# Optimization experiments

Measured on AMD Instinct MI355X. Metric: run time of the kernel, lower is better.

The kernel has to match this reference:

```python
import jax, jax.numpy as jnp
import numpy as np

VOL_DIM = 256  # stored volume is [256,256,256,1]


def _deform(c, W1, b1, W2, b2, W3, b3, Wf, bf):
    # chain of 1x1x1 convs (== per-voxel matmuls) with cos activations, residual *5
    h = jnp.cos(jnp.einsum('...c,cd->...d', c, W1) + b1)
    h = jnp.cos(jnp.einsum('...c,cd->...d', h, W2) + b2)
    h = jnp.cos(jnp.einsum('...c,cd->...d', h, W3) + b3)
    return c + 5.0 * (jnp.einsum('...c,cd->...d', h, Wf) + bf)


def _trilinear_sample(vol, coords):
    # vol: [X,Y,Z,C]; coords: [...,3] in voxel units (identity nifti edges)
    X, Y, Z, _ = vol.shape
    hi = jnp.array([X - 1, Y - 1, Z - 1], dtype=coords.dtype)
    c = jnp.clip(coords, 0.0, hi)
    c0 = jnp.floor(c)
    f = c - c0
    i0 = c0.astype(jnp.int32)
    i1 = jnp.minimum(i0 + 1, jnp.array([X - 1, Y - 1, Z - 1], jnp.int32))
    x0, y0, z0 = i0[..., 0], i0[..., 1], i0[..., 2]
    x1, y1, z1 = i1[..., 0], i1[..., 1], i1[..., 2]
    fx, fy, fz = f[..., 0:1], f[..., 1:2], f[..., 2:3]
    gx, gy, gz = 1.0 - fx, 1.0 - fy, 1.0 - fz
    out = (vol[x0, y0, z0] * (gx * gy * gz) + vol[x1, y0, z0] * (fx * gy * gz)
         + vol[x0, y1, z0] * (gx * fy * gz) + vol[x0, y0, z1] * (gx * gy * fz)
         + vol[x1, y1, z0] * (fx * fy * gz) + vol[x1, y0, z1] * (fx * gy * fz)
         + vol[x0, y1, z1] * (gx * fy * fz) + vol[x1, y1, z1] * (fx * fy * fz))
    return out  # [...,C]


def setup_inputs() -> dict:
    key = jax.random.key(0)
    ks = jax.random.split(key, 12)
    B, P = 64, 32
    # coords in [0, 255] world==voxel units; extra intensity channel (unused by call)
    coords = jax.random.uniform(ks[0], (B, P, P, P, 3), jnp.float32) * (VOL_DIM - 1.0)
    inten = jax.random.normal(ks[1], (B, P, P, P, 1), jnp.float32)
    x = jnp.concatenate([coords, inten], axis=-1)
    s = 0.1
    return {
        'x': x,
        'W1': jax.random.normal(ks[2], (3, 32), jnp.float32) * s,
        'b1': jax.random.normal(ks[3], (32,), jnp.float32) * s,
        'W2': jax.random.normal(ks[4], (32, 32), jnp.float32) * s,
        'b2': jax.random.normal(ks[5], (32,), jnp.float32) * s,
        'W3': jax.random.normal(ks[6], (32, 32), jnp.float32) * s,
        'b3': jax.random.normal(ks[7], (32,), jnp.float32) * s,
        'Wf': jax.random.normal(ks[8], (32, 3), jnp.float32) * s,
        'bf': jax.random.normal(ks[9], (3,), jnp.float32) * s,
        'vol': jax.random.normal(ks[10], (VOL_DIM, VOL_DIM, VOL_DIM, 1), jnp.float32),
    }


def reference(x, W1, b1, W2, b2, W3, b3, Wf, bf, vol):
    c = x[..., 0:3]                                   # world coords
    c = _deform(c, W1, b1, W2, b2, W3, b3, Wf, bf)    # deformed coords
    return _trilinear_sample(vol, c)                  # [B,32,32,32,1]
```

## Files before the change

kernel.cpp:

```cpp
#include <hip/hip_runtime.h>


#define NPTS (64 * 32 * 32 * 32)
#define NBLK64 (NPTS / 64)
#define NBLK (NPTS / 256)
#define SSTR 40

#define BXN 86
#define BYN 128
#define BZN 86
#define NBRICK (BXN * BYN * BZN)
#define RETILE_T (NBRICK * 8)
#define RETILE_BLK (RETILE_T / 256)
#define HALO_BYTES ((size_t)NBRICK * 64)

#define NBRICK_F (86 * 256 * 86)
#define RETILE2_T (NBRICK_F * 4)
#define RETILE2_BLK (RETILE2_T / 256)
#define FULL_BYTES ((size_t)NBRICK_F * 64)
#define WPREP_BYTES 4096

typedef __attribute__((ext_vector_type(8))) short bf16x8;
typedef __attribute__((ext_vector_type(8))) _Float16 h16x8;
typedef __attribute__((ext_vector_type(4))) short s16x4;
typedef __attribute__((ext_vector_type(4))) float f32x4;
typedef __attribute__((ext_vector_type(2))) unsigned long long u64x2;
typedef __attribute__((ext_vector_type(2))) unsigned uint2v;
typedef __attribute__((ext_vector_type(4))) unsigned uint4v;
typedef unsigned long long u64;
typedef unsigned short u16;

__device__ __forceinline__ short bf16rne(float f) {
    unsigned u = __builtin_bit_cast(unsigned, f);
    return (short)((u + 0x7fffu + ((u >> 16) & 1u)) >> 16);
}
__device__ __forceinline__ float bf16tof(short s) {
    return __builtin_bit_cast(float, ((unsigned)(unsigned short)s) << 16);
}
__device__ __forceinline__ float h2f(u16 h) {
    return (float)__builtin_bit_cast(_Float16, h);
}
__device__ __forceinline__ u16 f2h(float f) {
    return __builtin_bit_cast(u16, (_Float16)f);
}
__device__ __forceinline__ unsigned pk_h16(float a, float b) {
    return (unsigned)f2h(a) | ((unsigned)f2h(b) << 16);
}

__global__ __launch_bounds__(256)
void retile_k(const float4* __restrict__ vol, u64* __restrict__ dst) {
    int t   = blockIdx.x * 256 + threadIdx.x;
    int q   = t & 7;
    int gz  = (t >> 3) & 63;
    int gyx = t >> 9;
    int x = ((gyx >> 7) << 2) + (q >> 1);
    int y = ((gyx & 127) << 1) + (q & 1);
    float4 v = vol[(((x << 8) + y) << 6) + gz];
    u64 r =  (u64)f2h(v.x)
          | ((u64)f2h(v.y) << 16)
          | ((u64)f2h(v.z) << 32)
          | ((u64)f2h(v.w) << 48);
    dst[t] = r;
}

__global__ __launch_bounds__(256)
void retile_halo_k(const float* __restrict__ vol, u64* __restrict__ dst) {
    int t  = blockIdx.x * 256 + threadIdx.x;
    int q  = t & 7;
    int b  = t >> 3;
    int bz = (int)((unsigned)b % 86u);
    int r  = (int)((unsigned)b / 86u);
    int by = r & 127;
    int bx = r >> 7;
    int x  = min(bx * 3 + (q >> 1), 255);
    int y  = (by << 1) + (q & 1);
    int z0 = bz * 3;
    const float* row = vol + (((x << 8) + y) << 8);
    float v0 = row[z0];
    float v1 = row[min(z0 + 1, 255)];
    float v2 = row[min(z0 + 2, 255)];
    float v3 = row[min(z0 + 3, 255)];
    u64 rr = (u64)f2h(v0)
          | ((u64)f2h(v1) << 16)
          | ((u64)f2h(v2) << 32)
          | ((u64)f2h(v3) << 48);
    dst[t] = rr;
}

__global__ __launch_bounds__(256)
void retile_full2_k(const float* __restrict__ vol, u64* __restrict__ dst,
                    const float* __restrict__ W2, const float* __restrict__ W3,
                    short* __restrict__ wsW) {
    int t  = blockIdx.x * 256 + threadIdx.x;
    int dx = t & 3;
    int b  = t >> 2;
    int bz = (int)((unsigned)b % 86u);
    int r  = (int)((unsigned)b / 86u);
    int by = r & 255;
    int bx = r >> 8;
    int x  = min(bx * 3 + dx, 255);
    int y1 = min(by + 1, 255);
    int z0 = bz * 3;
    int zl = (z0 > 252) ? 252 : z0;
    const float* row0 = vol + (((x << 8) + by) << 8) + zl;
    const float* row1 = vol + (((x << 8) + y1) << 8) + zl;
    float va[4], vb[4];
    __builtin_memcpy(va, row0, 16);
    __builtin_memcpy(vb, row1, 16);
    if (z0 == 255) {
        va[0] = va[1] = va[2] = va[3];
        vb[0] = vb[1] = vb[2] = vb[3];
    }
    u64 lo = (u64)f2h(va[0]) | ((u64)f2h(va[1]) << 16)
           | ((u64)f2h(va[2]) << 32) | ((u64)f2h(va[3]) << 48);
    u64 hi = (u64)f2h(vb[0]) | ((u64)f2h(vb[1]) << 16)
           | ((u64)f2h(vb[2]) << 32) | ((u64)f2h(vb[3]) << 48);
    u64x2 st; st.x = lo; st.y = hi;
    *(u64x2*)(dst + (b << 3) + (dx << 1)) = st;

    if (blockIdx.x == 0) {
        int tt = threadIdx.x;
        #pragma unroll
        for (int e0 = 0; e0 < 2048; e0 += 256) {
            int e = e0 + tt;
            int ly  = e >> 10, half = (e >> 9) & 1, ln = (e >> 3) & 63, j = e & 7;
            int qq  = ln >> 4, mm = ln & 15;
            const float* W = ly ? W3 : W2;
            wsW[e] = (short)f2h(W[(qq * 8 + j) * 32 + half * 16 + mm]);
        }
    }
}

__global__ __launch_bounds__(64, 8)
void deform3d_k(const float4* __restrict__ x,
                const float4* __restrict__ W1,
                const float4* __restrict__ b1,
                const float*  __restrict__ b2,
                const float*  __restrict__ b3,
                const float*  __restrict__ Wf,
                const float*  __restrict__ bf_,
                const u64*    __restrict__ volh,
                const short*  __restrict__ wsW,
                float* __restrict__ out)
{
    __shared__ short L[64 * SSTR];
    const int lane = threadIdx.x;
    const int m16  = lane & 15;
    const int q    = lane >> 4;

    const int p = blockIdx.x * 64 + lane;

    const float4 xv = x[p];
    const float c0 = xv.x, c1 = xv.y, c2 = xv.z;

    {
        unsigned hw[4];
        #pragma unroll
        for (int j4 = 0; j4 < 8; ++j4) {
            float4 wa = W1[j4], wb = W1[8 + j4], wc = W1[16 + j4], bb = b1[j4];
            float v0 = __cosf(fmaf(c0, wa.x, fmaf(c1, wb.x, fmaf(c2, wc.x, bb.x))));
            float v1 = __cosf(fmaf(c0, wa.y, fmaf(c1, wb.y, fmaf(c2, wc.y, bb.y))));
            float v2 = __cosf(fmaf(c0, wa.z, fmaf(c1, wb.z, fmaf(c2, wc.z, bb.z))));
            float v3 = __cosf(fmaf(c0, wa.w, fmaf(c1, wb.w, fmaf(c2, wc.w, bb.w))));
            int o = (j4 & 1) * 2;
            hw[o + 0] = pk_h16(v0, v1);
            hw[o + 1] = pk_h16(v2, v3);
            if (j4 & 1) {
                uint4v st; st.x = hw[0]; st.y = hw[1]; st.z = hw[2]; st.w = hw[3];
                *(uint4v*)&L[lane * SSTR + (j4 - 1) * 4] = st;
            }
        }
    }
    __syncthreads();

    const bf16x8* __restrict__ wA = (const bf16x8*)wsW;

    {
        h16x8 A0 = __builtin_bit_cast(h16x8, wA[lane]);
        h16x8 A1 = __builtin_bit_cast(h16x8, wA[64 + lane]);
        const float4 blo = *(const float4*)&b2[q * 4];
        const float4 bhi = *(const float4*)&b2[16 + q * 4];
        #pragma unroll
        for (int t = 0; t < 4; ++t) {
            h16x8 bfrag = __builtin_bit_cast(h16x8,
                *(const bf16x8*)&L[(t * 16 + m16) * SSTR + q * 8]);
            f32x4 z = { 0.f, 0.f, 0.f, 0.f };
            f32x4 d0 = __builtin_amdgcn_mfma_f32_16x16x32_f16(A0, bfrag, z, 0, 0, 0);
            f32x4 d1 = __builtin_amdgcn_mfma_f32_16x16x32_f16(A1, bfrag, z, 0, 0, 0);
            unsigned a0 = pk_h16(__cosf(d0[0] + blo.x), __cosf(d0[1] + blo.y));
            unsigned a1 = pk_h16(__cosf(d0[2] + blo.z), __cosf(d0[3] + blo.w));
            unsigned a2 = pk_h16(__cosf(d1[0] + bhi.x), __cosf(d1[1] + bhi.y));
            unsigned a3 = pk_h16(__cosf(d1[2] + bhi.z), __cosf(d1[3] + bhi.w));
            uint2v s0; s0.x = a0; s0.y = a1;
            uint2v s1; s1.x = a2; s1.y = a3;
            *(uint2v*)&L[(t * 16 + m16) * SSTR + q * 4]      = s0;
            *(uint2v*)&L[(t * 16 + m16) * SSTR + 16 + q * 4] = s1;
        }
        __syncthreads();
    }

    float acc0 = 0.f, acc1 = 0.f, acc2 = 0.f;
    {
        h16x8 A0 = __builtin_bit_cast(h16x8, wA[128 + lane]);
        h16x8 A1 = __builtin_bit_cast(h16x8, wA[192 + lane]);
        const float4 blo = *(const float4*)&b3[q * 4];
        const float4 bhi = *(const float4*)&b3[16 + q * 4];
        const float bl[4] = { blo.x, blo.y, blo.z, blo.w };
        const float bh[4] = { bhi.x, bhi.y, bhi.z, bhi.w };
        float wf[8][3];
        #pragma unroll
        for (int r = 0; r < 4; ++r) {
            #pragma unroll
            for (int c = 0; c < 3; ++c) {
                wf[r][c]     = Wf[(q * 4 + r) * 3 + c];
                wf[4 + r][c] = Wf[(16 + q * 4 + r) * 3 + c];
            }
        }
        #pragma unroll
        for (int t = 0; t < 4; ++t) {
            h16x8 bfrag = __builtin_bit_cast(h16x8,
                *(const bf16x8*)&L[(t * 16 + m16) * SSTR + q * 8]);
            f32x4 z = { 0.f, 0.f, 0.f, 0.f };
            f32x4 d0 = __builtin_amdgcn_mfma_f32_16x16x32_f16(A0, bfrag, z, 0, 0, 0);
            f32x4 d1 = __builtin_amdgcn_mfma_f32_16x16x32_f16(A1, bfrag, z, 0, 0, 0);
            float s0 = 0.f, s1 = 0.f, s2 = 0.f;
            #pragma unroll
            for (int r = 0; r < 4; ++r) {
                float h = __cosf(d0[r] + bl[r]);
                s0 = fmaf(h, wf[r][0], s0);
                s1 = fmaf(h, wf[r][1], s1);
                s2 = fmaf(h, wf[r][2], s2);
                float h2 = __cosf(d1[r] + bh[r]);
                s0 = fmaf(h2, wf[4 + r][0], s0);
                s1 = fmaf(h2, wf[4 + r][1], s1);
                s2 = fmaf(h2, wf[4 + r][2], s2);
            }
            s0 += __shfl_xor(s0, 16); s0 += __shfl_xor(s0, 32);
            s1 += __shfl_xor(s1, 16); s1 += __shfl_xor(s1, 32);
            s2 += __shfl_xor(s2, 16); s2 += __shfl_xor(s2, 32);
            if (q == t) { acc0 = s0; acc1 = s1; acc2 = s2; }
        }
    }
    float e0 = fmaf(5.f, acc0 + bf_[0], c0);
    float e1 = fmaf(5.f, acc1 + bf_[1], c1);
    float e2 = fmaf(5.f, acc2 + bf_[2], c2);

    e0 = fminf(fmaxf(e0, 0.f), 255.f);
    e1 = fminf(fmaxf(e1, 0.f), 255.f);
    e2 = fminf(fmaxf(e2, 0.f), 255.f);
    float fl0 = floorf(e0), fl1 = floorf(e1), fl2 = floorf(e2);
    float fx = e0 - fl0, fy = e1 - fl1, fz = e2 - fl2;
    float gx = 1.f - fx, gy = 1.f - fy, gz = 1.f - fz;
    int x0 = (int)fl0, y0 = (int)fl1, z0 = (int)fl2;

    int bx = (int)((unsigned)x0 / 3u);  int lx = x0 - bx * 3;
    int bz = (int)((unsigned)z0 / 3u);  int lz = z0 - bz * 3;
    const u64* g = volh + ((((bx << 8) + y0) * 86 + bz) << 3) + (lx << 1);
    u64 g0 = g[0];
    u64 g1 = g[1];
    u64 g2 = g[2];
    u64 g3 = g[3];
    const int sh = lz * 16;
    u64 s0 = g0 >> sh, s1 = g1 >> sh, s2 = g2 >> sh, s3 = g3 >> sh;
    float v000 = h2f((u16)s0), v001 = h2f((u16)(s0 >> 16));
    float v010 = h2f((u16)s1), v011 = h2f((u16)(s1 >> 16));
    float v100 = h2f((u16)s2), v101 = h2f((u16)(s2 >> 16));
    float v110 = h2f((u16)s3), v111 = h2f((u16)(s3 >> 16));

    float r = gz * (gy * (gx*v000 + fx*v100) + fy * (gx*v010 + fx*v110))
            + fz * (gy * (gx*v001 + fx*v101) + fy * (gx*v011 + fx*v111));

    out[p] = r;
}

template <int MODE>
__global__ __launch_bounds__(256, 8)
void deform_sample_k(const float4* __restrict__ x,
                     const float4* __restrict__ W1,
                     const float4* __restrict__ b1,
                     const float*  __restrict__ W2,
                     const float*  __restrict__ b2,
                     const float*  __restrict__ W3,
                     const float*  __restrict__ b3,
                     const float*  __restrict__ Wf,
                     const float*  __restrict__ bf_,
                     const float*  __restrict__ volf,
                     const u64*    __restrict__ volh,
                     float* __restrict__ out)
{
    __shared__ short lds[4 * 64 * SSTR];
    const int tid  = threadIdx.x;
    const int lane = tid & 63;
    const int wv   = tid >> 6;
    const int m16  = lane & 15;
    const int q    = lane >> 4;
    short* __restrict__ L = &lds[wv * 64 * SSTR];

    const int p = blockIdx.x * 256 + tid;

    const float4 xv = x[p];
    const float c0 = xv.x, c1 = xv.y, c2 = xv.z;

    {
        bf16x8 hw;
        #pragma unroll
        for (int j4 = 0; j4 < 8; ++j4) {
            float4 wa = W1[j4], wb = W1[8 + j4], wc = W1[16 + j4], bb = b1[j4];
            float v0 = __cosf(fmaf(c0, wa.x, fmaf(c1, wb.x, fmaf(c2, wc.x, bb.x))));
            float v1 = __cosf(fmaf(c0, wa.y, fmaf(c1, wb.y, fmaf(c2, wc.y, bb.y))));
            float v2 = __cosf(fmaf(c0, wa.z, fmaf(c1, wb.z, fmaf(c2, wc.z, bb.z))));
            float v3 = __cosf(fmaf(c0, wa.w, fmaf(c1, wb.w, fmaf(c2, wc.w, bb.w))));
            int o = (j4 & 1) * 4;
            hw[o+0] = bf16rne(v0); hw[o+1] = bf16rne(v1);
            hw[o+2] = bf16rne(v2); hw[o+3] = bf16rne(v3);
            if (j4 & 1)
                *(bf16x8*)&L[lane * SSTR + (j4 - 1) * 4] = hw;
        }
    }
    __syncthreads();

    const float* const Wly[2] = { W2, W3 };
    const float* const bly[2] = { b2, b3 };
    #pragma unroll
    for (int ly = 0; ly < 2; ++ly) {
        const float* __restrict__ W  = Wly[ly];
        const float* __restrict__ bb = bly[ly];
        bf16x8 A0, A1;
        #pragma unroll
        for (int j = 0; j < 8; ++j) {
            A0[j] = bf16rne(W[(q * 8 + j) * 32 + m16]);
            A1[j] = bf16rne(W[(q * 8 + j) * 32 + 16 + m16]);
        }
        const float4 blo = *(const float4*)&bb[q * 4];
        const float4 bhi = *(const float4*)&bb[16 + q * 4];

        #pragma unroll
        for (int t = 0; t < 4; ++t) {
            bf16x8 bfrag = *(const bf16x8*)&L[(t * 16 + m16) * SSTR + q * 8];
            f32x4 z = { 0.f, 0.f, 0.f, 0.f };
            f32x4 d0 = __builtin_amdgcn_mfma_f32_16x16x32_bf16(A0, bfrag, z, 0, 0, 0);
            f32x4 d1 = __builtin_amdgcn_mfma_f32_16x16x32_bf16(A1, bfrag, z, 0, 0, 0);

            s16x4 w0, w1;
            w0[0] = bf16rne(__cosf(d0[0] + blo.x));
            w0[1] = bf16rne(__cosf(d0[1] + blo.y));
            w0[2] = bf16rne(__cosf(d0[2] + blo.z));
            w0[3] = bf16rne(__cosf(d0[3] + blo.w));
            w1[0] = bf16rne(__cosf(d1[0] + bhi.x));
            w1[1] = bf16rne(__cosf(d1[1] + bhi.y));
            w1[2] = bf16rne(__cosf(d1[2] + bhi.z));
            w1[3] = bf16rne(__cosf(d1[3] + bhi.w));
            *(s16x4*)&L[(t * 16 + m16) * SSTR + q * 4]      = w0;
            *(s16x4*)&L[(t * 16 + m16) * SSTR + 16 + q * 4] = w1;
        }
        __syncthreads();
    }

    float d0 = bf_[0], d1 = bf_[1], d2 = bf_[2];
    #pragma unroll
    for (int j4 = 0; j4 < 8; ++j4) {
        s16x4 v = *(const s16x4*)&L[lane * SSTR + j4 * 4];
        #pragma unroll
        for (int r = 0; r < 4; ++r) {
            float hv = bf16tof(v[r]);
            int ii = j4 * 4 + r;
            d0 = fmaf(hv, Wf[3*ii+0], d0);
            d1 = fmaf(hv, Wf[3*ii+1], d1);
            d2 = fmaf(hv, Wf[3*ii+2], d2);
        }
    }
    float e0 = fmaf(5.f, d0, c0);
    float e1 = fmaf(5.f, d1, c1);
    float e2 = fmaf(5.f, d2, c2);

    e0 = fminf(fmaxf(e0, 0.f), 255.f);
    e1 = fminf(fmaxf(e1, 0.f), 255.f);
    e2 = fminf(fmaxf(e2, 0.f), 255.f);
    float fl0 = floorf(e0), fl1 = floorf(e1), fl2 = floorf(e2);
    float fx = e0 - fl0, fy = e1 - fl1, fz = e2 - fl2;
    float gx = 1.f - fx, gy = 1.f - fy, gz = 1.f - fz;
    int x0 = (int)fl0, y0 = (int)fl1, z0 = (int)fl2;
    int x1 = min(x0 + 1, 255), y1 = min(y0 + 1, 255), z1 = min(z0 + 1, 255);

    float v000, v001, v010, v011, v100, v101, v110, v111;

    if constexpr (MODE == 3) {
        int bx = (int)((unsigned)x0 / 3u);  int lx = x0 - bx * 3;
        int bz = (int)((unsigned)z0 / 3u);  int lz = z0 - bz * 3;
        const u64* g = volh + ((((bx << 8) + y0) * 86 + bz) << 3) + (lx << 1);
        u64 g0 = g[0];
        u64 g1 = g[1];
        u64 g2 = g[2];
        u64 g3 = g[3];
        const int sh = lz * 16;
        u64 s0 = g0 >> sh, s1 = g1 >> sh, s2 = g2 >> sh, s3 = g3 >> sh;
        v000 = h2f((u16)s0);  v001 = h2f((u16)(s0 >> 16));
        v010 = h2f((u16)s1);  v011 = h2f((u16)(s1 >> 16));
        v100 = h2f((u16)s2);  v101 = h2f((u16)(s2 >> 16));
        v110 = h2f((u16)s3);  v111 = h2f((u16)(s3 >> 16));
    } else if constexpr (MODE == 2) {
        int bx = (int)((unsigned)x0 / 3u);  int lx = x0 - bx * 3;
        int by = y0 >> 1;                   int ly = y0 & 1;
        int bz = (int)((unsigned)z0 / 3u);  int lz = z0 - bz * 3;
        const char* vb = (const char*)volh;
        const int lineA = ((((bx << 7) + by) * 86) + bz) << 6;
        const int byB   = min(by + 1, 127);
        const int lineB = (ly == 0) ? lineA
                                    : (((((bx << 7) + byB) * 86) + bz) << 6);
        const int yrowB = (ly == 0) ? 1 : ((y0 == 255) ? 1 : 0);
        const int offA  = lx * 16 + ly * 8;
        const int offB  = lx * 16 + yrowB * 8;
        u64 LA0 = *(const u64*)(vb + lineA + offA);
        u64 LA1 = *(const u64*)(vb + lineA + offA + 16);
        u64 LB0 = *(const u64*)(vb + lineB + offB);
        u64 LB1 = *(const u64*)(vb + lineB + offB + 16);
        const int sh = lz * 16;
        u64 sA0 = LA0 >> sh, sA1 = LA1 >> sh, sB0 = LB0 >> sh, sB1 = LB1 >> sh;
        v000 = h2f((u16)sA0);  v001 = h2f((u16)(sA0 >> 16));
        v100 = h2f((u16)sA1);  v101 = h2f((u16)(sA1 >> 16));
        v010 = h2f((u16)sB0);  v011 = h2f((u16)(sB0 >> 16));
        v110 = h2f((u16)sB1);  v111 = h2f((u16)(sB1 >> 16));
    } else if constexpr (MODE == 1) {
        const int lz  = z0 & 3;
        const int zp  = (z0 >> 2) << 6;
        const int xp0 = ((x0 >> 2) << 19) | ((x0 & 3) << 4);
        const int xp1 = ((x1 >> 2) << 19) | ((x1 & 3) << 4);
        const int yp0 = ((y0 >> 1) << 12) | ((y0 & 1) << 3);
        const int yp1 = ((y1 >> 1) << 12) | ((y1 & 1) << 3);
        const char* vb = (const char*)volh;
        const int a00 = xp0 | yp0 | zp, a10 = xp1 | yp0 | zp;
        const int a01 = xp0 | yp1 | zp, a11 = xp1 | yp1 | zp;
        u64 L00 = *(const u64*)(vb + a00);
        u64 L10 = *(const u64*)(vb + a10);
        u64 L01 = *(const u64*)(vb + a01);
        u64 L11 = *(const u64*)(vb + a11);
        u64 H00 = 0, H10 = 0, H01 = 0, H11 = 0;
        const bool crossz = (lz == 3) && (z0 < 255);
        if (crossz) {
            H00 = *(const u64*)(vb + a00 + 64);
            H10 = *(const u64*)(vb + a10 + 64);
            H01 = *(const u64*)(vb + a01 + 64);
            H11 = *(const u64*)(vb + a11 + 64);
        }
        const int sh = lz * 16;
        const bool in_line = (lz < 3);
        auto ext = [&](u64 lo, u64 hi, float& a, float& b) {
            u64 s = lo >> sh;
            a = h2f((u16)s);
            float b_in = h2f((u16)(s >> 16));
            float b_nx = h2f((u16)hi);
            b = in_line ? b_in : (crossz ? b_nx : a);
        };
        ext(L00, H00, v000, v001);
        ext(L10, H10, v100, v101);
        ext(L01, H01, v010, v011);
        ext(L11, H11, v110, v111);
    } else {
        int b00 = (x0 << 16) | (y0 << 8);
        int b01 = (x0 << 16) | (y1 << 8);
        int b10 = (x1 << 16) | (y0 << 8);
        int b11 = (x1 << 16) | (y1 << 8);
        v000 = volf[b00 + z0]; v001 = volf[b00 + z1];
        v010 = volf[b01 + z0]; v011 = volf[b01 + z1];
        v100 = volf[b10 + z0]; v101 = volf[b10 + z1];
        v110 = volf[b11 + z0]; v111 = volf[b11 + z1];
    }

    float r = gz * (gy * (gx*v000 + fx*v100) + fy * (gx*v010 + fx*v110))
            + fz * (gy * (gx*v001 + fx*v101) + fy * (gx*v011 + fx*v111));

    out[p] = r;
}

extern "C" void kernel_launch(void* const* d_in, const int* in_sizes, int n_in,
                              void* d_out, int out_size, void* d_ws, size_t ws_size,
                              hipStream_t stream) {
    const float4* x   = (const float4*)d_in[0];
    const float4* W1  = (const float4*)d_in[1];
    const float4* b1  = (const float4*)d_in[2];
    const float*  W2  = (const float*)d_in[3];
    const float*  b2  = (const float*)d_in[4];
    const float*  W3  = (const float*)d_in[5];
    const float*  b3  = (const float*)d_in[6];
    const float*  Wf  = (const float*)d_in[7];
    const float*  bf_ = (const float*)d_in[8];
    const float*  vol = (const float*)d_in[9];
    float* out = (float*)d_out;

    const size_t needF = FULL_BYTES + WPREP_BYTES;
    const size_t needH = HALO_BYTES;
    const size_t need1 = (size_t)4194304 * 8;

    if (ws_size >= needF) {
        u64*   volh = (u64*)d_ws;
        short* wsW  = (short*)((char*)d_ws + FULL_BYTES);
        retile_full2_k<<<RETILE2_BLK, 256, 0, stream>>>(vol, volh, W2, W3, wsW);
        deform3d_k<<<NBLK64, 64, 0, stream>>>(x, W1, b1, b2, b3, Wf, bf_,
                                              volh, wsW, out);
    } else if (ws_size >= needH) {
        u64* volh = (u64*)d_ws;
        retile_halo_k<<<RETILE_BLK, 256, 0, stream>>>(vol, volh);
        deform_sample_k<2><<<NBLK, 256, 0, stream>>>(x, W1, b1, W2, b2, W3, b3,
                                                     Wf, bf_, nullptr, volh, out);
    } else if (ws_size >= need1) {
        u64* volh = (u64*)d_ws;
        retile_k<<<16384, 256, 0, stream>>>((const float4*)vol, volh);
        deform_sample_k<1><<<NBLK, 256, 0, stream>>>(x, W1, b1, W2, b2, W3, b3,
                                                     Wf, bf_, nullptr, volh, out);
    } else {
        deform_sample_k<0><<<NBLK, 256, 0, stream>>>(x, W1, b1, W2, b2, W3, b3,
                                                     Wf, bf_, vol, nullptr, out);
    }
}
```

Measured before the change: 206.2 us.

## Process two point groups per wavefront to overlap volume gathers with MLP

```diff
diff --git a/kernel.cpp b/kernel.cpp
--- a/kernel.cpp
+++ b/kernel.cpp
@@ -2,7 +2,7 @@
 
 
 #define NPTS (64 * 32 * 32 * 32)
-#define NBLK64 (NPTS / 64)
+#define NBLK128 (NPTS / 128)
 #define NBLK (NPTS / 256)
 #define SSTR 40
 
@@ -132,7 +132,7 @@
 }
 
 __global__ __launch_bounds__(64, 8)
-void deform3d_k(const float4* __restrict__ x,
+void deform3e_k(const float4* __restrict__ x,
                 const float4* __restrict__ W1,
                 const float4* __restrict__ b1,
                 const float*  __restrict__ b2,
@@ -148,129 +148,148 @@
     const int m16  = lane & 15;
     const int q    = lane >> 4;
 
-    const int p = blockIdx.x * 64 + lane;
-
-    const float4 xv = x[p];
-    const float c0 = xv.x, c1 = xv.y, c2 = xv.z;
-
-    {
-        unsigned hw[4];
-        #pragma unroll
-        for (int j4 = 0; j4 < 8; ++j4) {
-            float4 wa = W1[j4], wb = W1[8 + j4], wc = W1[16 + j4], bb = b1[j4];
-            float v0 = __cosf(fmaf(c0, wa.x, fmaf(c1, wb.x, fmaf(c2, wc.x, bb.x))));
-            float v1 = __cosf(fmaf(c0, wa.y, fmaf(c1, wb.y, fmaf(c2, wc.y, bb.y))));
-            float v2 = __cosf(fmaf(c0, wa.z, fmaf(c1, wb.z, fmaf(c2, wc.z, bb.z))));
-            float v3 = __cosf(fmaf(c0, wa.w, fmaf(c1, wb.w, fmaf(c2, wc.w, bb.w))));
-            int o = (j4 & 1) * 2;
-            hw[o + 0] = pk_h16(v0, v1);
-            hw[o + 1] = pk_h16(v2, v3);
-            if (j4 & 1) {
-                uint4v st; st.x = hw[0]; st.y = hw[1]; st.z = hw[2]; st.w = hw[3];
-                *(uint4v*)&L[lane * SSTR + (j4 - 1) * 4] = st;
+    const int p0 = blockIdx.x * 128 + lane;
+    const int p1 = p0 + 64;
+
+    const bf16x8* __restrict__ wA = (const bf16x8*)wsW;
+
+    const float4 xv0 = x[p0];
+    const float4 xv1 = x[p1];
+
+    auto lds_fence = [] { asm volatile("s_waitcnt lgkmcnt(0)" ::: "memory"); };
+
+    auto mlp = [&](float c0, float c1, float c2,
+                   float& e0, float& e1, float& e2) {
+        lds_fence();
+        {
+            unsigned hw[4];
+            #pragma unroll
+            for (int j4 = 0; j4 < 8; ++j4) {
+                float4 wa = W1[j4], wb = W1[8 + j4], wc = W1[16 + j4], bb = b1[j4];
+                float v0 = __cosf(fmaf(c0, wa.x, fmaf(c1, wb.x, fmaf(c2, wc.x, bb.x))));
+                float v1 = __cosf(fmaf(c0, wa.y, fmaf(c1, wb.y, fmaf(c2, wc.y, bb.y))));
+                float v2 = __cosf(fmaf(c0, wa.z, fmaf(c1, wb.z, fmaf(c2, wc.z, bb.z))));
+                float v3 = __cosf(fmaf(c0, wa.w, fmaf(c1, wb.w, fmaf(c2, wc.w, bb.w))));
+                int o = (j4 & 1) * 2;
+                hw[o + 0] = pk_h16(v0, v1);
+                hw[o + 1] = pk_h16(v2, v3);
+                if (j4 & 1) {
+                    uint4v st; st.x = hw[0]; st.y = hw[1]; st.z = hw[2]; st.w = hw[3];
+                    *(uint4v*)&L[lane * SSTR + (j4 - 1) * 4] = st;
+                }
             }
         }
-    }
-    __syncthreads();
-
-    const bf16x8* __restrict__ wA = (const bf16x8*)wsW;
-
-    {
-        h16x8 A0 = __builtin_bit_cast(h16x8, wA[lane]);
-        h16x8 A1 = __builtin_bit_cast(h16x8, wA[64 + lane]);
-        const float4 blo = *(const float4*)&b2[q * 4];
-        const float4 bhi = *(const float4*)&b2[16 + q * 4];
-        #pragma unroll
-        for (int t = 0; t < 4; ++t) {
-            h16x8 bfrag = __builtin_bit_cast(h16x8,
-                *(const bf16x8*)&L[(t * 16 + m16) * SSTR + q * 8]);
-            f32x4 z = { 0.f, 0.f, 0.f, 0.f };
-            f32x4 d0 = __builtin_amdgcn_mfma_f32_16x16x32_f16(A0, bfrag, z, 0, 0, 0);
-            f32x4 d1 = __builtin_amdgcn_mfma_f32_16x16x32_f16(A1, bfrag, z, 0, 0, 0);
-            unsigned a0 = pk_h16(__cosf(d0[0] + blo.x), __cosf(d0[1] + blo.y));
-            unsigned a1 = pk_h16(__cosf(d0[2] + blo.z), __cosf(d0[3] + blo.w));
-            unsigned a2 = pk_h16(__cosf(d1[0] + bhi.x), __cosf(d1[1] + bhi.y));
-            unsigned a3 = pk_h16(__cosf(d1[2] + bhi.z), __cosf(d1[3] + bhi.w));
-            uint2v s0; s0.x = a0; s0.y = a1;
-            uint2v s1; s1.x = a2; s1.y = a3;
-            *(uint2v*)&L[(t * 16 + m16) * SSTR + q * 4]      = s0;
-            *(uint2v*)&L[(t * 16 + m16) * SSTR + 16 + q * 4] = s1;
-        }
-        __syncthreads();
-    }
-
-    float acc0 = 0.f, acc1 = 0.f, acc2 = 0.f;
-    {
-        h16x8 A0 = __builtin_bit_cast(h16x8, wA[128 + lane]);
-        h16x8 A1 = __builtin_bit_cast(h16x8, wA[192 + lane]);
-        const float4 blo = *(const float4*)&b3[q * 4];
-        const float4 bhi = *(const float4*)&b3[16 + q * 4];
-        const float bl[4] = { blo.x, blo.y, blo.z, blo.w };
-        const float bh[4] = { bhi.x, bhi.y, bhi.z, bhi.w };
-        float wf[8][3];
-        #pragma unroll
-        for (int r = 0; r < 4; ++r) {
+        lds_fence();
+        {
+            h16x8 A0 = __builtin_bit_cast(h16x8, wA[lane]);
+            h16x8 A1 = __builtin_bit_cast(h16x8, wA[64 + lane]);
+            const float4 blo = *(const float4*)&b2[q * 4];
+            const float4 bhi = *(const float4*)&b2[16 + q * 4];
             #pragma unroll
-            for (int c = 0; c < 3; ++c) {
-                wf[r][c]     = Wf[(q * 4 + r) * 3 + c];
-                wf[4 + r][c] = Wf[(16 + q * 4 + r) * 3 + c];
+            for (int t = 0; t < 4; ++t) {
+                h16x8 bfrag = __builtin_bit_cast(h16x8,
+                    *(const bf16x8*)&L[(t * 16 + m16) * SSTR + q * 8]);
+                f32x4 z = { 0.f, 0.f, 0.f, 0.f };
+                f32x4 d0 = __builtin_amdgcn_mfma_f32_16x16x32_f16(A0, bfrag, z, 0, 0, 0);
+                f32x4 d1 = __builtin_amdgcn_mfma_f32_16x16x32_f16(A1, bfrag, z, 0, 0, 0);
+                unsigned a0 = pk_h16(__cosf(d0[0] + blo.x), __cosf(d0[1] + blo.y));
+                unsigned a1 = pk_h16(__cosf(d0[2] + blo.z), __cosf(d0[3] + blo.w));
+                unsigned a2 = pk_h16(__cosf(d1[0] + bhi.x), __cosf(d1[1] + bhi.y));
+                unsigned a3 = pk_h16(__cosf(d1[2] + bhi.z), __cosf(d1[3] + bhi.w));
+                uint2v s0; s0.x = a0; s0.y = a1;
+                uint2v s1; s1.x = a2; s1.y = a3;
+                *(uint2v*)&L[(t * 16 + m16) * SSTR + q * 4]      = s0;
+                *(uint2v*)&L[(t * 16 + m16) * SSTR + 16 + q * 4] = s1;
             }
         }
-        #pragma unroll
-        for (int t = 0; t < 4; ++t) {
-            h16x8 bfrag = __builtin_bit_cast(h16x8,
-                *(const bf16x8*)&L[(t * 16 + m16) * SSTR + q * 8]);
-            f32x4 z = { 0.f, 0.f, 0.f, 0.f };
-            f32x4 d0 = __builtin_amdgcn_mfma_f32_16x16x32_f16(A0, bfrag, z, 0, 0, 0);
-            f32x4 d1 = __builtin_amdgcn_mfma_f32_16x16x32_f16(A1, bfrag, z, 0, 0, 0);
-            float s0 = 0.f, s1 = 0.f, s2 = 0.f;
+        lds_fence();
+        float acc0 = 0.f, acc1 = 0.f, acc2 = 0.f;
+        {
+            h16x8 A0 = __builtin_bit_cast(h16x8, wA[128 + lane]);
+            h16x8 A1 = __builtin_bit_cast(h16x8, wA[192 + lane]);
+            const float4 blo = *(const float4*)&b3[q * 4];
+            const float4 bhi = *(const float4*)&b3[16 + q * 4];
+            const float bl[4] = { blo.x, blo.y, blo.z, blo.w };
+            const float bh[4] = { bhi.x, bhi.y, bhi.z, bhi.w };
+            float wf[8][3];
             #pragma unroll
             for (int r = 0; r < 4; ++r) {
-                float h = __cosf(d0[r] + bl[r]);
-                s0 = fmaf(h, wf[r][0], s0);
-                s1 = fmaf(h, wf[r][1], s1);
-                s2 = fmaf(h, wf[r][2], s2);
-                float h2 = __cosf(d1[r] + bh[r]);
-                s0 = fmaf(h2, wf[4 + r][0], s0);
-                s1 = fmaf(h2, wf[4 + r][1], s1);
-                s2 = fmaf(h2, wf[4 + r][2], s2);
+                #pragma unroll
+                for (int c = 0; c < 3; ++c) {
+                    wf[r][c]     = Wf[(q * 4 + r) * 3 + c];
+                    wf[4 + r][c] = Wf[(16 + q * 4 + r) * 3 + c];
+                }
             }
-            s0 += __shfl_xor(s0, 16); s0 += __shfl_xor(s0, 32);
-            s1 += __shfl_xor(s1, 16); s1 += __shfl_xor(s1, 32);
-            s2 += __shfl_xor(s2, 16); s2 += __shfl_xor(s2, 32);
-            if (q == t) { acc0 = s0; acc1 = s1; acc2 = s2; }
-        }
-    }
-    float e0 = fmaf(5.f, acc0 + bf_[0], c0);
-    float e1 = fmaf(5.f, acc1 + bf_[1], c1);
-    float e2 = fmaf(5.f, acc2 + bf_[2], c2);
-
-    e0 = fminf(fmaxf(e0, 0.f), 255.f);
-    e1 = fminf(fmaxf(e1, 0.f), 255.f);
-    e2 = fminf(fmaxf(e2, 0.f), 255.f);
-    float fl0 = floorf(e0), fl1 = floorf(e1), fl2 = floorf(e2);
-    float fx = e0 - fl0, fy = e1 - fl1, fz = e2 - fl2;
-    float gx = 1.f - fx, gy = 1.f - fy, gz = 1.f - fz;
-    int x0 = (int)fl0, y0 = (int)fl1, z0 = (int)fl2;
-
-    int bx = (int)((unsigned)x0 / 3u);  int lx = x0 - bx * 3;
-    int bz = (int)((unsigned)z0 / 3u);  int lz = z0 - bz * 3;
-    const u64* g = volh + ((((bx << 8) + y0) * 86 + bz) << 3) + (lx << 1);
-    u64 g0 = g[0];
-    u64 g1 = g[1];
-    u64 g2 = g[2];
-    u64 g3 = g[3];
-    const int sh = lz * 16;
-    u64 s0 = g0 >> sh, s1 = g1 >> sh, s2 = g2 >> sh, s3 = g3 >> sh;
-    float v000 = h2f((u16)s0), v001 = h2f((u16)(s0 >> 16));
-    float v010 = h2f((u16)s1), v011 = h2f((u16)(s1 >> 16));
-    float v100 = h2f((u16)s2), v101 = h2f((u16)(s2 >> 16));
-    float v110 = h2f((u16)s3), v111 = h2f((u16)(s3 >> 16));
-
-    float r = gz * (gy * (gx*v000 + fx*v100) + fy * (gx*v010 + fx*v110))
-            + fz * (gy * (gx*v001 + fx*v101) + fy * (gx*v011 + fx*v111));
-
-    out[p] = r;
+            #pragma unroll
+            for (int t = 0; t < 4; ++t) {
+                h16x8 bfrag = __builtin_bit_cast(h16x8,
+                    *(const bf16x8*)&L[(t * 16 + m16) * SSTR + q * 8]);
+                f32x4 z = { 0.f, 0.f, 0.f, 0.f };
+                f32x4 d0 = __builtin_amdgcn_mfma_f32_16x16x32_f16(A0, bfrag, z, 0, 0, 0);
+                f32x4 d1 = __builtin_amdgcn_mfma_f32_16x16x32_f16(A1, bfrag, z, 0, 0, 0);
+                float s0 = 0.f, s1 = 0.f, s2 = 0.f;
+                #pragma unroll
+                for (int r = 0; r < 4; ++r) {
+                    float h = __cosf(d0[r] + bl[r]);
+                    s0 = fmaf(h, wf[r][0], s0);
+                    s1 = fmaf(h, wf[r][1], s1);
+                    s2 = fmaf(h, wf[r][2], s2);
+                    float h2 = __cosf(d1[r] + bh[r]);
+                    s0 = fmaf(h2, wf[4 + r][0], s0);
+                    s1 = fmaf(h2, wf[4 + r][1], s1);
+                    s2 = fmaf(h2, wf[4 + r][2], s2);
+                }
+                s0 += __shfl_xor(s0, 16); s0 += __shfl_xor(s0, 32);
+                s1 += __shfl_xor(s1, 16); s1 += __shfl_xor(s1, 32);
+                s2 += __shfl_xor(s2, 16); s2 += __shfl_xor(s2, 32);
+                if (q == t) { acc0 = s0; acc1 = s1; acc2 = s2; }
+            }
+        }
+        e0 = fmaf(5.f, acc0 + bf_[0], c0);
+        e1 = fmaf(5.f, acc1 + bf_[1], c1);
+        e2 = fmaf(5.f, acc2 + bf_[2], c2);
+    };
+
+    auto addr = [&](float e0, float e1, float e2,
+                    float& fx, float& fy, float& fz, int& sh) -> const u64* {
+        e0 = fminf(fmaxf(e0, 0.f), 255.f);
+        e1 = fminf(fmaxf(e1, 0.f), 255.f);
+        e2 = fminf(fmaxf(e2, 0.f), 255.f);
+        float fl0 = floorf(e0), fl1 = floorf(e1), fl2 = floorf(e2);
+        fx = e0 - fl0; fy = e1 - fl1; fz = e2 - fl2;
+        int x0 = (int)fl0, y0 = (int)fl1, z0 = (int)fl2;
+        int bx = (int)((unsigned)x0 / 3u);  int lx = x0 - bx * 3;
+        int bz = (int)((unsigned)z0 / 3u);  int lz = z0 - bz * 3;
+        sh = lz * 16;
+        return volh + ((((bx << 8) + y0) * 86 + bz) << 3) + (lx << 1);
+    };
+
+    auto interp = [](u64 g0, u64 g1, u64 g2, u64 g3,
+                     float fx, float fy, float fz, int sh) -> float {
+        float gx = 1.f - fx, gy = 1.f - fy, gz = 1.f - fz;
+        u64 s0 = g0 >> sh, s1 = g1 >> sh, s2 = g2 >> sh, s3 = g3 >> sh;
+        float v000 = h2f((u16)s0), v001 = h2f((u16)(s0 >> 16));
+        float v010 = h2f((u16)s1), v011 = h2f((u16)(s1 >> 16));
+        float v100 = h2f((u16)s2), v101 = h2f((u16)(s2 >> 16));
+        float v110 = h2f((u16)s3), v111 = h2f((u16)(s3 >> 16));
+        return gz * (gy * (gx*v000 + fx*v100) + fy * (gx*v010 + fx*v110))
+             + fz * (gy * (gx*v001 + fx*v101) + fy * (gx*v011 + fx*v111));
+    };
+
+    float e0A, e1A, e2A;
+    mlp(xv0.x, xv0.y, xv0.z, e0A, e1A, e2A);
+    float fxA, fyA, fzA; int shA;
+    const u64* gA = addr(e0A, e1A, e2A, fxA, fyA, fzA, shA);
+    u64 a0 = gA[0], a1 = gA[1], a2 = gA[2], a3 = gA[3];
+
+    float e0B, e1B, e2B;
+    mlp(xv1.x, xv1.y, xv1.z, e0B, e1B, e2B);
+    float fxB, fyB, fzB; int shB;
+    const u64* gB = addr(e0B, e1B, e2B, fxB, fyB, fzB, shB);
+    u64 b0 = gB[0], b1v = gB[1], b2v = gB[2], b3v = gB[3];
+
+    out[p0] = interp(a0, a1, a2, a3, fxA, fyA, fzA, shA);
+    out[p1] = interp(b0, b1v, b2v, b3v, fxB, fyB, fzB, shB);
 }
 
 template <int MODE>
@@ -495,8 +514,8 @@
         u64*   volh = (u64*)d_ws;
         short* wsW  = (short*)((char*)d_ws + FULL_BYTES);
         retile_full2_k<<<RETILE2_BLK, 256, 0, stream>>>(vol, volh, W2, W3, wsW);
-        deform3d_k<<<NBLK64, 64, 0, stream>>>(x, W1, b1, b2, b3, Wf, bf_,
-                                              volh, wsW, out);
+        deform3e_k<<<NBLK128, 64, 0, stream>>>(x, W1, b1, b2, b3, Wf, bf_,
+                                               volh, wsW, out);
     } else if (ws_size >= needH) {
         u64* volh = (u64*)d_ws;
         retile_halo_k<<<RETILE_BLK, 256, 0, stream>>>(vol, volh);
```

Result: slower. 231.9 us (+12.5%).
